# Kernel optimization log

Hardware: AMD Instinct MI355X
Metric: run time of the kernel (lower is better)

Reference implementation:

```python
import jax, jax.numpy as jnp
import numpy as np

FEATURES = 1024
HEAD_DIM = 64
NUM_HEADS = 16
EPS = 1e-5


def setup_inputs() -> dict:
    key = jax.random.key(0)
    ks = jax.random.split(key, 6)
    x = jax.random.normal(ks[0], (2, 2048, FEATURES), dtype=jnp.float32)
    s_in = 1.0 / np.sqrt(FEATURES)
    s_hd = 1.0 / np.sqrt(NUM_HEADS * HEAD_DIM)
    return {
        "x": x,
        "gamma": jnp.ones((FEATURES,), jnp.float32),
        "beta": jnp.zeros((FEATURES,), jnp.float32),
        "Wq": jax.random.normal(ks[1], (FEATURES, NUM_HEADS * HEAD_DIM), jnp.float32) * s_in,
        "Wkv": jax.random.normal(ks[2], (FEATURES, 2 * HEAD_DIM), jnp.float32) * s_in,
        "Wo": jax.random.normal(ks[3], (NUM_HEADS * HEAD_DIM, FEATURES), jnp.float32) * s_hd,
        "bo": jax.random.normal(ks[4], (FEATURES,), jnp.float32) * s_hd,
    }


def reference(x, gamma, beta, Wq, Wkv, Wo, bo):
    # LayerNorm over last dim
    mu = jnp.mean(x, axis=-1, keepdims=True)
    var = jnp.mean(jnp.square(x - mu), axis=-1, keepdims=True)
    xn = (x - mu) * jax.lax.rsqrt(var + EPS) * gamma + beta

    b, t, _ = x.shape
    q = (xn @ Wq).reshape(b, t, NUM_HEADS, HEAD_DIM).transpose(0, 2, 1, 3)  # b h t d
    kv = xn @ Wkv  # b s 2d
    k, v = kv[..., :HEAD_DIM], kv[..., HEAD_DIM:]  # b s d (single shared head)

    scale = HEAD_DIM ** (-0.5)
    attn = jnp.einsum('bhtd,bsd->bhts', q, k) * scale
    attn = jax.nn.softmax(attn, axis=-1)
    out = jnp.einsum('bhts,bsd->bhtd', attn, v)
    out = out.transpose(0, 2, 1, 3).reshape(b, t, NUM_HEADS * HEAD_DIM)
    return out @ Wo + bo + x
```

## Files before the change

### kernel.cpp

```cpp
#include <hip/hip_runtime.h>

typedef __attribute__((ext_vector_type(8))) __bf16 bf16x8;
typedef __attribute__((ext_vector_type(4))) float floatx4;
typedef unsigned short u16;
typedef unsigned int u32;

#define KSCALE 0.18033688011112042f

__device__ __forceinline__ u16 f2bf(float f) {
    union { float f; u32 u; } v; v.f = f;
    u32 r = v.u + 0x7fffu + ((v.u >> 16) & 1u);
    return (u16)(r >> 16);
}

__device__ __forceinline__ u32 pk2bf(float a, float b) {
    union { float f; u32 u; } x, y; x.f = a; y.f = b;
    return __builtin_amdgcn_perm(y.u + 0x8000u, x.u + 0x8000u, 0x07060302);
}

__device__ __forceinline__ void gl_lds16(const u16* g, u16* l) {
    __builtin_amdgcn_global_load_lds((const __attribute__((address_space(1))) void*)g,
                                     (__attribute__((address_space(3))) void*)l, 16, 0, 0);
}

__global__ __launch_bounds__(256) void prep(const float* __restrict__ Wq, const float* __restrict__ Wkv,
                                            const float* __restrict__ Wo, const float* __restrict__ x,
                                            const float* __restrict__ gamma, const float* __restrict__ beta,
                                            u16* __restrict__ WqkvT, u16* __restrict__ WoT,
                                            u16* __restrict__ xn) {
    __shared__ float tile[64][68];
    __shared__ float ps[4], ps2[4];
    const int bx = blockIdx.x;
    const int t = threadIdx.x;
    if (bx < 768) {
        const int z = bx >> 8, rem = bx & 255;
        const int tr = (rem >> 4) * 64, tc = (rem & 15) * 64;
        const float* in = (z == 0) ? Wq : (z == 1 ? Wkv : Wo);
        u16* out = (z == 0) ? WqkvT : (z == 1 ? WqkvT + (size_t)1024 * 1024 : WoT);
        const int cols = (z == 1) ? 128 : 1024;
        if (tc >= cols) return;
        for (int p = 0; p < 4; p++) {
            int ri = (t >> 4) + p * 16;
            int ci = (t & 15) * 4;
            float4 v = *(const float4*)&in[(size_t)(tr + ri) * cols + tc + ci];
            tile[ri][ci + 0] = v.x; tile[ri][ci + 1] = v.y;
            tile[ri][ci + 2] = v.z; tile[ri][ci + 3] = v.w;
        }
        __syncthreads();
        for (int p = 0; p < 4; p++) {
            int oc = (t >> 4) + p * 16;
            int ir = (t & 15) * 4;
            float s = (z == 1 && (tc + oc) < 64) ? KSCALE : 1.0f;
            ushort4 o;
            o.x = f2bf(tile[ir + 0][oc] * s);
            o.y = f2bf(tile[ir + 1][oc] * s);
            o.z = f2bf(tile[ir + 2][oc] * s);
            o.w = f2bf(tile[ir + 3][oc] * s);
            *(ushort4*)&out[(size_t)(tc + oc) * 1024 + tr + ir] = o;
        }
    } else {
        const int row = bx - 768;
        const float* xr = x + (size_t)row * 1024;
        float4 v = *(const float4*)&xr[t * 4];
        float s = v.x + v.y + v.z + v.w;
        float s2 = v.x * v.x + v.y * v.y + v.z * v.z + v.w * v.w;
        for (int off = 1; off < 64; off <<= 1) {
            s += __shfl_xor(s, off, 64);
            s2 += __shfl_xor(s2, off, 64);
        }
        int w = t >> 6, lane = t & 63;
        if (lane == 0) { ps[w] = s; ps2[w] = s2; }
        __syncthreads();
        float S = ps[0] + ps[1] + ps[2] + ps[3];
        float S2 = ps2[0] + ps2[1] + ps2[2] + ps2[3];
        float mu = S * (1.0f / 1024.0f);
        float var = S2 * (1.0f / 1024.0f) - mu * mu;
        float rstd = rsqrtf(var + 1e-5f);
        ushort4 o;
        o.x = f2bf((v.x - mu) * rstd * gamma[t * 4 + 0] + beta[t * 4 + 0]);
        o.y = f2bf((v.y - mu) * rstd * gamma[t * 4 + 1] + beta[t * 4 + 1]);
        o.z = f2bf((v.z - mu) * rstd * gamma[t * 4 + 2] + beta[t * 4 + 2]);
        o.w = f2bf((v.w - mu) * rstd * gamma[t * 4 + 3] + beta[t * 4 + 3]);
        *(ushort4*)&xn[(size_t)row * 1024 + t * 4] = o;
    }
}

template <bool FINAL>
__global__ __launch_bounds__(256) void gemm_bt(const u16* __restrict__ A, const u16* __restrict__ BT,
                                               u16* __restrict__ Cb, float* __restrict__ Cf,
                                               const float* __restrict__ bias, const float* __restrict__ resid,
                                               u16* __restrict__ vt2, int M, int N, int K) {
    __shared__ u16 as_[64 * 64];
    __shared__ u16 bs_[128 * 64];
    const int t = threadIdx.x;
    const int w = t >> 6, lane = t & 63, q = lane >> 4, c = lane & 15;
    const int tm = blockIdx.y * 64, tn = blockIdx.x * 128;
    const int wm = (w & 1) * 32, wn = (w >> 1) * 64;

    const int l3 = lane >> 3, sch = lane & 7;
    const int arow = w * 16 + l3;
    const int aswz = (sch ^ (arow & 7)) * 8;
    const int brow = w * 32 + l3;
    const int bswz = (sch ^ (brow & 7)) * 8;
    const u16* ag0 = A + (size_t)(tm + arow) * K + aswz;
    const u16* ag1 = ag0 + (size_t)8 * K;
    const u16* bg0 = BT + (size_t)(tn + brow) * K + bswz;
    const u16* bg1 = bg0 + (size_t)8 * K;
    const u16* bg2 = bg0 + (size_t)16 * K;
    const u16* bg3 = bg0 + (size_t)24 * K;
    u16* al0 = as_ + (w * 16) * 64;
    u16* al1 = as_ + (w * 16 + 8) * 64;
    u16* bl0 = bs_ + (w * 32) * 64;
    u16* bl1 = bs_ + (w * 32 + 8) * 64;
    u16* bl2 = bs_ + (w * 32 + 16) * 64;
    u16* bl3 = bs_ + (w * 32 + 24) * 64;

    floatx4 acc[2][4];
    for (int i = 0; i < 2; i++)
        for (int j = 0; j < 4; j++) acc[i][j] = (floatx4){0.f, 0.f, 0.f, 0.f};

    const int c7 = c & 7;
    for (int k0 = 0; k0 < K; k0 += 64) {
        __syncthreads();
        gl_lds16(ag0 + k0, al0);
        gl_lds16(ag1 + k0, al1);
        gl_lds16(bg0 + k0, bl0);
        gl_lds16(bg1 + k0, bl1);
        gl_lds16(bg2 + k0, bl2);
        gl_lds16(bg3 + k0, bl3);
        __syncthreads();
        bf16x8 af[2][2], bf[4][2];
#pragma unroll
        for (int i = 0; i < 2; i++)
#pragma unroll
            for (int kk = 0; kk < 2; kk++)
                af[i][kk] = *(const bf16x8*)&as_[(wm + i * 16 + c) * 64 + (((kk * 4 + q) ^ c7) * 8)];
#pragma unroll
        for (int j = 0; j < 4; j++)
#pragma unroll
            for (int kk = 0; kk < 2; kk++)
                bf[j][kk] = *(const bf16x8*)&bs_[(wn + j * 16 + c) * 64 + (((kk * 4 + q) ^ c7) * 8)];
#pragma unroll
        for (int kk = 0; kk < 2; kk++)
#pragma unroll
            for (int i = 0; i < 2; i++)
#pragma unroll
                for (int j = 0; j < 4; j++)
                    acc[i][j] = __builtin_amdgcn_mfma_f32_16x16x32_bf16(af[i][kk], bf[j][kk], acc[i][j], 0, 0, 0);
    }
#pragma unroll
    for (int i = 0; i < 2; i++)
#pragma unroll
        for (int j = 0; j < 4; j++)
#pragma unroll
            for (int r = 0; r < 4; r++) {
                int row = tm + wm + i * 16 + q * 4 + r;
                int col = tn + wn + j * 16 + c;
                float v = acc[i][j][r];
                if (FINAL) {
                    Cf[(size_t)row * N + col] = v + bias[col] + resid[(size_t)row * N + col];
                } else if (col < 1088) {
                    Cb[(size_t)row * N + col] = f2bf(v);
                } else {
                    int d = col - 1088;
                    int bb = row >> 11, sl = row & 2047;
                    int Bk = sl >> 5, u = sl & 31;
                    int up = ((u >> 2) & 3) * 8 + ((u >> 4) << 2) + (u & 3);
                    vt2[((size_t)(bb * 64 + d)) * 2048 + Bk * 32 + up] = f2bf(v);
                }
            }
}

union Vf { bf16x8 v; u32 w[4]; };

__global__ __launch_bounds__(256, 2) void attn7(const u16* __restrict__ qkv, const u16* __restrict__ vt2,
                                                u16* __restrict__ out) {
    __shared__ u16 ksm[2][64 * 64];
    __shared__ u16 vsm[2][64 * 64];
    const int t = threadIdx.x;
    const int w = t >> 6, lane = t & 63;
    const int q = lane >> 4, c = lane & 15;
    const int qt = blockIdx.x, hg = blockIdx.y, b = blockIdx.z;
    const int h = hg * 4 + w;
    const size_t qrow0 = (size_t)b * 2048 + qt * 32;
    const u16* kbase = qkv + (size_t)b * 2048 * 1152 + 1024;
    const u16* vbase = vt2 + (size_t)b * 64 * 2048;

    const int l3 = lane >> 3, sch = lane & 7;
    const int srow = w * 16 + l3;
    const int swz = (sch ^ (srow & 7)) * 8;
    const u16* kg0 = kbase + (size_t)srow * 1152 + swz;
    const u16* kg1 = kg0 + (size_t)8 * 1152;
    const u16* vg0 = vbase + (size_t)srow * 2048 + swz;
    const u16* vg1 = vg0 + (size_t)8 * 2048;
    u16* kl0[2] = {&ksm[0][(w * 16) * 64], &ksm[1][(w * 16) * 64]};
    u16* kl1[2] = {&ksm[0][(w * 16 + 8) * 64], &ksm[1][(w * 16 + 8) * 64]};
    u16* vl0[2] = {&vsm[0][(w * 16) * 64], &vsm[1][(w * 16) * 64]};
    u16* vl1[2] = {&vsm[0][(w * 16 + 8) * 64], &vsm[1][(w * 16 + 8) * 64]};

    bf16x8 qf[2][2];
#pragma unroll
    for (int mi = 0; mi < 2; mi++)
#pragma unroll
        for (int kk = 0; kk < 2; kk++)
            qf[mi][kk] = *(const bf16x8*)&qkv[(qrow0 + mi * 16 + c) * 1152 + h * 64 + kk * 32 + q * 8];

    floatx4 O[4][2], Lacc[2];
#pragma unroll
    for (int di = 0; di < 4; di++)
#pragma unroll
        for (int mi = 0; mi < 2; mi++) O[di][mi] = (floatx4){0.f, 0.f, 0.f, 0.f};
    Lacc[0] = (floatx4){0.f, 0.f, 0.f, 0.f};
    Lacc[1] = (floatx4){0.f, 0.f, 0.f, 0.f};
    Vf ones;
    ones.w[0] = ones.w[1] = ones.w[2] = ones.w[3] = 0x3F803F80u;

    gl_lds16(kg0, kl0[0]);
    gl_lds16(kg1, kl1[0]);
    gl_lds16(vg0, vl0[0]);
    gl_lds16(vg1, vl1[0]);
    __syncthreads();

    const int c7 = c & 7;
    for (int tt = 0; tt < 32; tt++) {
        const int cur = tt & 1, nxt = cur ^ 1;
        if (tt < 31) {
            const size_t ko = (size_t)(tt + 1) * 64 * 1152;
            const int vo = (tt + 1) * 64;
            gl_lds16(kg0 + ko, kl0[nxt]);
            gl_lds16(kg1 + ko, kl1[nxt]);
            gl_lds16(vg0 + vo, vl0[nxt]);
            gl_lds16(vg1 + vo, vl1[nxt]);
        }

        bf16x8 kf[4][2];
        Vf vf[4][2];
#pragma unroll
        for (int ni = 0; ni < 4; ni++)
#pragma unroll
            for (int kk = 0; kk < 2; kk++)
                kf[ni][kk] = *(const bf16x8*)&ksm[cur][(ni * 16 + c) * 64 + (((kk * 4 + q) ^ c7) * 8)];
#pragma unroll
        for (int di = 0; di < 4; di++)
#pragma unroll
            for (int kk = 0; kk < 2; kk++)
                vf[di][kk].v = *(const bf16x8*)&vsm[cur][(di * 16 + c) * 64 + (((kk * 4 + q) ^ c7) * 8)];

        floatx4 sacc[4][2];
#pragma unroll
        for (int ni = 0; ni < 4; ni++)
#pragma unroll
            for (int mi = 0; mi < 2; mi++) {
                floatx4 z = (floatx4){0.f, 0.f, 0.f, 0.f};
                z = __builtin_amdgcn_mfma_f32_16x16x32_bf16(kf[ni][0], qf[mi][0], z, 0, 0, 0);
                z = __builtin_amdgcn_mfma_f32_16x16x32_bf16(kf[ni][1], qf[mi][1], z, 0, 0, 0);
                sacc[ni][mi] = z;
            }

        u32 pk[4][2][2];
#pragma unroll
        for (int mi = 0; mi < 2; mi++)
#pragma unroll
            for (int ni = 0; ni < 4; ni++) {
                float p0 = exp2f(sacc[ni][mi][0]);
                float p1 = exp2f(sacc[ni][mi][1]);
                float p2 = exp2f(sacc[ni][mi][2]);
                float p3 = exp2f(sacc[ni][mi][3]);
                pk[ni][mi][0] = pk2bf(p0, p1);
                pk[ni][mi][1] = pk2bf(p2, p3);
            }

#pragma unroll
        for (int kk = 0; kk < 2; kk++) {
            Vf pf[2];
#pragma unroll
            for (int mi = 0; mi < 2; mi++) {
                pf[mi].w[0] = pk[2 * kk][mi][0];
                pf[mi].w[1] = pk[2 * kk][mi][1];
                pf[mi].w[2] = pk[2 * kk + 1][mi][0];
                pf[mi].w[3] = pk[2 * kk + 1][mi][1];
            }
#pragma unroll
            for (int di = 0; di < 4; di++)
#pragma unroll
                for (int mi = 0; mi < 2; mi++)
                    O[di][mi] = __builtin_amdgcn_mfma_f32_16x16x32_bf16(vf[di][kk].v, pf[mi].v, O[di][mi], 0, 0, 0);
#pragma unroll
            for (int mi = 0; mi < 2; mi++)
                Lacc[mi] = __builtin_amdgcn_mfma_f32_16x16x32_bf16(ones.v, pf[mi].v, Lacc[mi], 0, 0, 0);
        }

        __syncthreads();
    }

    float inv[2] = {1.0f / Lacc[0][0], 1.0f / Lacc[1][0]};
#pragma unroll
    for (int di = 0; di < 4; di++)
#pragma unroll
        for (int mi = 0; mi < 2; mi++) {
            ushort4 o;
            o.x = f2bf(O[di][mi][0] * inv[mi]);
            o.y = f2bf(O[di][mi][1] * inv[mi]);
            o.z = f2bf(O[di][mi][2] * inv[mi]);
            o.w = f2bf(O[di][mi][3] * inv[mi]);
            *(ushort4*)&out[(qrow0 + mi * 16 + c) * 1024 + h * 64 + di * 16 + q * 4] = o;
        }
}

extern "C" void kernel_launch(void* const* d_in, const int* in_sizes, int n_in,
                              void* d_out, int out_size, void* d_ws, size_t ws_size,
                              hipStream_t stream) {
    const float* x = (const float*)d_in[0];
    const float* gamma = (const float*)d_in[1];
    const float* beta = (const float*)d_in[2];
    const float* Wq = (const float*)d_in[3];
    const float* Wkv = (const float*)d_in[4];
    const float* Wo = (const float*)d_in[5];
    const float* bo = (const float*)d_in[6];
    float* out = (float*)d_out;

    u16* WqkvT = (u16*)d_ws;
    u16* WoT = WqkvT + (size_t)1152 * 1024;
    u16* xn = WoT + (size_t)1024 * 1024;
    u16* qkv = xn + (size_t)4096 * 1024;
    u16* vt2 = qkv + (size_t)4096 * 1152;
    u16* attnO = xn;

    prep<<<4864, 256, 0, stream>>>(Wq, Wkv, Wo, x, gamma, beta, WqkvT, WoT, xn);
    gemm_bt<false><<<dim3(9, 64), 256, 0, stream>>>(xn, WqkvT, qkv, nullptr, nullptr, nullptr, vt2,
                                                    4096, 1152, 1024);
    attn7<<<dim3(64, 4, 2), 256, 0, stream>>>(qkv, vt2, attnO);
    gemm_bt<true><<<dim3(8, 64), 256, 0, stream>>>(attnO, WoT, nullptr, out, bo, x, nullptr,
                                                   4096, 1024, 1024);
}
```

Before: 182.5 us.

## Fuse output projection into attention kernel via per-head atomic accumulation

Removes the separate output-projection GEMM. Each attention wave multiplies its normalized head output by a pre-swizzled bf16 slice of Wo held in MFMA fragment layout, then atomically adds the result into the fp32 output. The prep kernel now writes x+bo into the output as the initial value and builds the fragment-ordered Wo. This saves a kernel launch and the attention-output round trip through memory, but adds 16-way fp32 atomic contention per output element and a large volume of atomic traffic.

```diff
diff --git a/kernel.cpp b/kernel.cpp
--- a/kernel.cpp
+++ b/kernel.cpp
@@ -26,17 +26,18 @@
 __global__ __launch_bounds__(256) void prep(const float* __restrict__ Wq, const float* __restrict__ Wkv,
                                             const float* __restrict__ Wo, const float* __restrict__ x,
                                             const float* __restrict__ gamma, const float* __restrict__ beta,
-                                            u16* __restrict__ WqkvT, u16* __restrict__ WoT,
-                                            u16* __restrict__ xn) {
+                                            const float* __restrict__ bo,
+                                            u16* __restrict__ WqkvT, u16* __restrict__ woF,
+                                            u16* __restrict__ xn, float* __restrict__ out) {
     __shared__ float tile[64][68];
     __shared__ float ps[4], ps2[4];
     const int bx = blockIdx.x;
     const int t = threadIdx.x;
-    if (bx < 768) {
+    if (bx < 512) {
         const int z = bx >> 8, rem = bx & 255;
         const int tr = (rem >> 4) * 64, tc = (rem & 15) * 64;
-        const float* in = (z == 0) ? Wq : (z == 1 ? Wkv : Wo);
-        u16* out = (z == 0) ? WqkvT : (z == 1 ? WqkvT + (size_t)1024 * 1024 : WoT);
+        const float* in = (z == 0) ? Wq : Wkv;
+        u16* outw = (z == 0) ? WqkvT : WqkvT + (size_t)1024 * 1024;
         const int cols = (z == 1) ? 128 : 1024;
         if (tc >= cols) return;
         for (int p = 0; p < 4; p++) {
@@ -56,12 +57,33 @@
             o.y = f2bf(tile[ir + 1][oc] * s);
             o.z = f2bf(tile[ir + 2][oc] * s);
             o.w = f2bf(tile[ir + 3][oc] * s);
-            *(ushort4*)&out[(size_t)(tc + oc) * 1024 + tr + ir] = o;
+            *(ushort4*)&outw[(size_t)(tc + oc) * 1024 + tr + ir] = o;
+        }
+    } else if (bx < 528) {
+        const int h = bx - 512;
+        const int l = t & 63, sub = t >> 6;
+        const int ql = l >> 4, cl = l & 15;
+        u16* wf = woF + (size_t)h * 65536;
+        for (int nfb = 0; nfb < 16; nfb++) {
+            int nf = nfb * 4 + sub;
+            for (int kk = 0; kk < 2; kk++) {
+                u16 tmp[8];
+#pragma unroll
+                for (int j = 0; j < 8; j++) {
+                    int row = h * 64 + kk * 32 + (j >> 2) * 16 + ql * 4 + (j & 3);
+                    tmp[j] = f2bf(Wo[(size_t)row * 1024 + nf * 16 + cl]);
+                }
+                *(uint4*)&wf[(nf * 2 + kk) * 512 + l * 8] = *(uint4*)tmp;
+            }
         }
     } else {
-        const int row = bx - 768;
+        const int row = bx - 528;
         const float* xr = x + (size_t)row * 1024;
         float4 v = *(const float4*)&xr[t * 4];
+        float4 bo4 = *(const float4*)&bo[t * 4];
+        float4 of;
+        of.x = v.x + bo4.x; of.y = v.y + bo4.y; of.z = v.z + bo4.z; of.w = v.w + bo4.w;
+        *(float4*)&out[(size_t)row * 1024 + t * 4] = of;
         float s = v.x + v.y + v.z + v.w;
         float s2 = v.x * v.x + v.y * v.y + v.z * v.z + v.w * v.w;
         for (int off = 1; off < 64; off <<= 1) {
@@ -85,11 +107,8 @@
     }
 }
 
-template <bool FINAL>
-__global__ __launch_bounds__(256) void gemm_bt(const u16* __restrict__ A, const u16* __restrict__ BT,
-                                               u16* __restrict__ Cb, float* __restrict__ Cf,
-                                               const float* __restrict__ bias, const float* __restrict__ resid,
-                                               u16* __restrict__ vt2, int M, int N, int K) {
+__global__ __launch_bounds__(256) void gemm_qkv(const u16* __restrict__ A, const u16* __restrict__ BT,
+                                                u16* __restrict__ Cb, u16* __restrict__ vt2, int N, int K) {
     __shared__ u16 as_[64 * 64];
     __shared__ u16 bs_[128 * 64];
     const int t = threadIdx.x;
@@ -157,9 +176,7 @@
                 int row = tm + wm + i * 16 + q * 4 + r;
                 int col = tn + wn + j * 16 + c;
                 float v = acc[i][j][r];
-                if (FINAL) {
-                    Cf[(size_t)row * N + col] = v + bias[col] + resid[(size_t)row * N + col];
-                } else if (col < 1088) {
+                if (col < 1088) {
                     Cb[(size_t)row * N + col] = f2bf(v);
                 } else {
                     int d = col - 1088;
@@ -173,8 +190,8 @@
 
 union Vf { bf16x8 v; u32 w[4]; };
 
-__global__ __launch_bounds__(256, 2) void attn7(const u16* __restrict__ qkv, const u16* __restrict__ vt2,
-                                                u16* __restrict__ out) {
+__global__ __launch_bounds__(256, 2) void attn8(const u16* __restrict__ qkv, const u16* __restrict__ vt2,
+                                                const u16* __restrict__ woF, float* __restrict__ out) {
     __shared__ u16 ksm[2][64 * 64];
     __shared__ u16 vsm[2][64 * 64];
     const int t = threadIdx.x;
@@ -294,17 +311,31 @@
     }
 
     float inv[2] = {1.0f / Lacc[0][0], 1.0f / Lacc[1][0]};
-#pragma unroll
-    for (int di = 0; di < 4; di++)
+    Vf af[2][2];
+#pragma unroll
+    for (int mi = 0; mi < 2; mi++)
+#pragma unroll
+        for (int kk = 0; kk < 2; kk++) {
+            af[mi][kk].w[0] = pk2bf(O[2 * kk][mi][0] * inv[mi], O[2 * kk][mi][1] * inv[mi]);
+            af[mi][kk].w[1] = pk2bf(O[2 * kk][mi][2] * inv[mi], O[2 * kk][mi][3] * inv[mi]);
+            af[mi][kk].w[2] = pk2bf(O[2 * kk + 1][mi][0] * inv[mi], O[2 * kk + 1][mi][1] * inv[mi]);
+            af[mi][kk].w[3] = pk2bf(O[2 * kk + 1][mi][2] * inv[mi], O[2 * kk + 1][mi][3] * inv[mi]);
+        }
+    const u16* wf = woF + (size_t)h * 65536;
+#pragma unroll 4
+    for (int nf = 0; nf < 64; nf++) {
+        bf16x8 bf0 = *(const bf16x8*)&wf[(nf * 2 + 0) * 512 + lane * 8];
+        bf16x8 bf1 = *(const bf16x8*)&wf[(nf * 2 + 1) * 512 + lane * 8];
 #pragma unroll
         for (int mi = 0; mi < 2; mi++) {
-            ushort4 o;
-            o.x = f2bf(O[di][mi][0] * inv[mi]);
-            o.y = f2bf(O[di][mi][1] * inv[mi]);
-            o.z = f2bf(O[di][mi][2] * inv[mi]);
-            o.w = f2bf(O[di][mi][3] * inv[mi]);
-            *(ushort4*)&out[(qrow0 + mi * 16 + c) * 1024 + h * 64 + di * 16 + q * 4] = o;
-        }
+            floatx4 acc = (floatx4){0.f, 0.f, 0.f, 0.f};
+            acc = __builtin_amdgcn_mfma_f32_16x16x32_bf16(af[mi][0].v, bf0, acc, 0, 0, 0);
+            acc = __builtin_amdgcn_mfma_f32_16x16x32_bf16(af[mi][1].v, bf1, acc, 0, 0, 0);
+#pragma unroll
+            for (int r = 0; r < 4; r++)
+                atomicAdd(&out[(qrow0 + mi * 16 + q * 4 + r) * 1024 + nf * 16 + c], acc[r]);
+        }
+    }
 }
 
 extern "C" void kernel_launch(void* const* d_in, const int* in_sizes, int n_in,
@@ -320,16 +351,12 @@
     float* out = (float*)d_out;
 
     u16* WqkvT = (u16*)d_ws;
-    u16* WoT = WqkvT + (size_t)1152 * 1024;
-    u16* xn = WoT + (size_t)1024 * 1024;
+    u16* woF = WqkvT + (size_t)1152 * 1024;
+    u16* xn = woF + (size_t)16 * 65536;
     u16* qkv = xn + (size_t)4096 * 1024;
     u16* vt2 = qkv + (size_t)4096 * 1152;
-    u16* attnO = xn;
-
-    prep<<<4864, 256, 0, stream>>>(Wq, Wkv, Wo, x, gamma, beta, WqkvT, WoT, xn);
-    gemm_bt<false><<<dim3(9, 64), 256, 0, stream>>>(xn, WqkvT, qkv, nullptr, nullptr, nullptr, vt2,
-                                                    4096, 1152, 1024);
-    attn7<<<dim3(64, 4, 2), 256, 0, stream>>>(qkv, vt2, attnO);
-    gemm_bt<true><<<dim3(8, 64), 256, 0, stream>>>(attnO, WoT, nullptr, out, bo, x, nullptr,
-                                                   4096, 1024, 1024);
-}
+
+    prep<<<4624, 256, 0, stream>>>(Wq, Wkv, Wo, x, gamma, beta, bo, WqkvT, woF, xn, out);
+    gemm_qkv<<<dim3(9, 64), 256, 0, stream>>>(xn, WqkvT, qkv, vt2, 1152, 1024);
+    attn8<<<dim3(64, 4, 2), 256, 0, stream>>>(qkv, vt2, woF, out);
+}
```

Measured after the change: 384.2 us. 111% more time.
